# Kernel optimization log

Hardware: AMD Instinct MI355X
Metric: run time of the kernel (lower is better)

The kernel has to match this reference:

```python
import jax, jax.numpy as jnp
import numpy as np

N = 20000      # nodes
E = 320000     # edges (avg degree 16)
DIN = 50       # PPI input features
C = 121        # PPI classes
HID = 1024     # 4 heads x 256 concatenated
H3 = 6         # heads in last layer


def setup_inputs() -> dict:
    key = jax.random.key(0)
    ks = jax.random.split(key, 7)
    X = jax.random.normal(ks[0], (N, DIN), jnp.float32)
    edge_index = jax.random.randint(ks[1], (2, E), 0, N, dtype=jnp.int32)
    def w(k, i, o):
        return jax.random.normal(k, (i, o), jnp.float32) / jnp.sqrt(jnp.float32(i))
    return {
        "X": X,
        "edge_index": edge_index,
        "W1": w(ks[2], DIN, HID),        # 4 heads x 256, concatenated
        "W2": w(ks[3], HID, HID),        # 4 heads x 256 GCN weights
        "S2": w(ks[4], HID, HID),        # 4 heads x 256 skip linears
        "W3": w(ks[5], HID, H3 * C),     # 6 heads x num_classes GCN weights
        "S3": w(ks[6], HID, H3 * C),     # 6 heads x num_classes skip linears
    }


def _agg(xw, row, col, norm, n):
    # GCN symmetric-normalized neighbor sum: out[col] += norm * xw[row]
    return jax.ops.segment_sum(xw[row] * norm[:, None], col, num_segments=n)


def reference(X, edge_index, W1, W2, S2, W3, S3):
    n = X.shape[0]
    row, col = edge_index[0], edge_index[1]
    # degree at targets (add_self_loops=False), D^{-1/2} A D^{-1/2} normalization
    deg = jax.ops.segment_sum(jnp.ones(row.shape, X.dtype), col, num_segments=n)
    dis = jnp.where(deg > 0, deg ** -0.5, 0.0)
    norm = dis[row] * dis[col]
    # layer 1: 4 GCN heads (weights concatenated), elu, concat
    h1 = jax.nn.elu(_agg(X @ W1, row, col, norm, n))              # [N, 1024]
    # layer 2: 4 GCN heads + linear skip, elu, concat
    h2 = jax.nn.elu(_agg(h1 @ W2, row, col, norm, n) + h1 @ S2)   # [N, 1024]
    # layer 3: 6 GCN heads + linear skip, average over heads (Identity act)
    y = _agg(h2 @ W3, row, col, norm, n) + h2 @ S3                # [N, 6*C]
    return y.reshape(n, H3, C).mean(axis=1)                       # [N, C]
```

## Files before the change

kernel.cpp:

```cpp
#include <hip/hip_runtime.h>
#include <hip/hip_bf16.h>
#include <math.h>

#define N_NODES 20000
#define N_EDGES 320000
#define DIN 50
#define HID 1024
#define NC3 726
#define NCLS 121
#define KCAT 2048
#define NQ 242

typedef __attribute__((ext_vector_type(8))) _Float16 half8;
typedef __attribute__((ext_vector_type(4))) float floatx4;

__device__ __forceinline__ unsigned short f2h(float v) {
    _Float16 h = (_Float16)v;
    return __builtin_bit_cast(unsigned short, h);
}
__device__ __forceinline__ float h2f(unsigned short u) {
    return (float)__builtin_bit_cast(_Float16, u);
}

__device__ __forceinline__ void async16(const void* g, void* l) {
    __builtin_amdgcn_global_load_lds(
        (const __attribute__((address_space(1))) void*)g,
        (__attribute__((address_space(3))) void*)l,
        16, 0, 0);
}


__global__ void zero_int_kernel(int* p, int n) {
    int i = blockIdx.x * blockDim.x + threadIdx.x;
    if (i < n) p[i] = 0;
}

__global__ __launch_bounds__(1024) void scan_kernel(const int* __restrict__ deg,
                                                    int* __restrict__ offs,
                                                    int* __restrict__ cursor,
                                                    float* __restrict__ dis,
                                                    int n, int total) {
    __shared__ int part[1024];
    int t = threadIdx.x;
    const int CH = (n + 1023) / 1024;
    int base0 = t * CH;
    int s = 0;
    for (int i = 0; i < CH; ++i) {
        int idx = base0 + i;
        if (idx < n) s += deg[idx];
    }
    part[t] = s;
    __syncthreads();
    for (int d = 1; d < 1024; d <<= 1) {
        int v = (t >= d) ? part[t - d] : 0;
        __syncthreads();
        part[t] += v;
        __syncthreads();
    }
    int run = part[t] - s;
    for (int i = 0; i < CH; ++i) {
        int idx = base0 + i;
        if (idx < n) {
            int d = deg[idx];
            offs[idx] = run;
            cursor[idx] = run;
            dis[idx] = d > 0 ? rsqrtf((float)d) : 0.0f;
            run += d;
        }
    }
    if (t == 1023) offs[n] = total;
}

__global__ void scatter_kernel(const int* __restrict__ row, const int* __restrict__ col,
                               const float* __restrict__ dis, int* __restrict__ cursor,
                               int* __restrict__ csr_src, float* __restrict__ csr_w, int e) {
    int i = blockIdx.x * blockDim.x + threadIdx.x;
    if (i < e) {
        int r = row[i], c = col[i];
        float nm = dis[r] * dis[c];
        int pos = atomicAdd(&cursor[c], 1);
        csr_src[pos] = r;
        csr_w[pos] = nm;
    }
}

__global__ __launch_bounds__(256) void prep_kernel(const int* __restrict__ ecol,
                                                   int* __restrict__ deg,
                                                   const float* __restrict__ W1,
                                                   unsigned short* __restrict__ Bt1,
                                                   const float* __restrict__ W2,
                                                   const float* __restrict__ S2,
                                                   unsigned short* __restrict__ Bt2,
                                                   const float* __restrict__ W3,
                                                   const float* __restrict__ S3,
                                                   unsigned short* __restrict__ Bt3) {
    __shared__ unsigned short tile[32][33];
    const int b = blockIdx.x;
    const int tid = threadIdx.x;

    if (b < 2048) {
        int src = b >> 10;
        int t = b & 1023;
        int k0 = (t >> 5) * 32;
        int n0 = (t & 31) * 32;
        const float* W = src ? S2 : W2;
        int koff = src ? HID : 0;
        int tx = tid & 31;
        int ty = tid >> 5;
#pragma unroll
        for (int r = 0; r < 32; r += 8)
            tile[ty + r][tx] = f2h(W[(size_t)(k0 + ty + r) * HID + n0 + tx]);
        __syncthreads();
#pragma unroll
        for (int r = 0; r < 32; r += 8)
            Bt2[(size_t)(n0 + ty + r) * KCAT + koff + k0 + tx] = tile[tx][ty + r];
    } else if (b < 2304) {
        int tb = b - 2048;
        int src = tb >> 7;
        int t = tb & 127;
        int k0 = (t >> 2) * 32;
        int c0 = (t & 3) * 32;
        const float* W = src ? S3 : W3;
        int tx = tid & 31;
        int ty = tid >> 5;
#pragma unroll
        for (int r = 0; r < 32; r += 8) {
            int k = k0 + ty + r, c = c0 + tx;
            float v = 0.0f;
            if (c < NCLS) {
                const float* p = W + (size_t)k * NC3 + c;
                v = (p[0] + p[121] + p[242] + p[363] + p[484] + p[605]) * (1.0f / 6.0f);
            }
            tile[ty + r][tx] = f2h(v);
        }
        __syncthreads();
#pragma unroll
        for (int r = 0; r < 32; r += 8) {
            int c = c0 + ty + r;
            if (c < NCLS)
                Bt3[(size_t)(src * NCLS + c) * HID + k0 + tx] = tile[tx][ty + r];
        }
    } else if (b < 2560) {
        int i = (b - 2304) * 256 + tid;
        int n = i / 64, k = i - n * 64;
        Bt1[i] = (k < DIN) ? f2h(W1[(size_t)k * HID + n]) : (unsigned short)0;
    } else {
        int i = (b - 2560) * 256 + tid;
        if (i < N_EDGES) atomicAdd(&deg[ecol[i]], 1);
    }
}


__global__ __launch_bounds__(64) void aggX_kernel(const float* __restrict__ X,
                                                  const int* __restrict__ offs,
                                                  const int* __restrict__ csr_src,
                                                  const float* __restrict__ csr_w,
                                                  unsigned short* __restrict__ gX) {
    int n = blockIdx.x;
    int t = threadIdx.x;
    float a = 0.0f;
    if (t < DIN) {
        int p0 = offs[n], p1 = offs[n + 1];
        for (int p = p0; p < p1; ++p) {
            a = fmaf(csr_w[p], X[(size_t)csr_src[p] * DIN + t], a);
        }
    }
    gX[(size_t)n * 64 + t] = (t < DIN) ? f2h(a) : (unsigned short)0;
}

__global__ __launch_bounds__(256) void agg_slice_kernel(const unsigned short* __restrict__ h,
                                                        const int* __restrict__ offs,
                                                        const int* __restrict__ csr_src,
                                                        const float* __restrict__ csr_w,
                                                        unsigned short* __restrict__ g) {
    const int f = blockIdx.x;
    const int slice = f & 7;
    const int nb = f >> 3;
    const int tid = threadIdx.x;
    const int n = nb * 16 + (tid >> 4);
    const int coloff = slice * 128 + (tid & 15) * 8;
    const unsigned short* hp = h + coloff;

    float a[8] = {0, 0, 0, 0, 0, 0, 0, 0};
    int p0 = offs[n], p1 = offs[n + 1];
    for (int p = p0; p < p1; ++p) {
        int s = csr_src[p];
        float w = csr_w[p];
        uint4 v = *(const uint4*)&hp[(size_t)s * HID];
        const unsigned short* vs = (const unsigned short*)&v;
#pragma unroll
        for (int j = 0; j < 8; ++j) a[j] = fmaf(w, h2f(vs[j]), a[j]);
    }
    unsigned short ov[8];
#pragma unroll
    for (int j = 0; j < 8; ++j) ov[j] = f2h(a[j]);
    *(uint4*)&g[(size_t)n * HID + coloff] = *(const uint4*)ov;
}

__global__ __launch_bounds__(256) void agg3_kernel(const unsigned short* __restrict__ Q,
                                                   const int* __restrict__ offs,
                                                   const int* __restrict__ csr_src,
                                                   const float* __restrict__ csr_w,
                                                   float* __restrict__ out) {
    int n = blockIdx.x * 2 + (threadIdx.x >> 7);
    int c = threadIdx.x & 127;
    if (c >= NCLS) return;
    float a = 0.0f;
    int p0 = offs[n], p1 = offs[n + 1];
    for (int p = p0; p < p1; ++p) {
        a = fmaf(csr_w[p], h2f(Q[(size_t)csr_src[p] * NQ + c]), a);
    }
    a += h2f(Q[(size_t)n * NQ + NCLS + c]);
    out[(size_t)n * NCLS + c] = a;
}


#define GBM 128
#define GBN 128
#define GBK 32

template <int EPI>
__global__ __launch_bounds__(256, 4) void mfma_gemm_kernel(
        const unsigned short* __restrict__ Ag, const unsigned short* __restrict__ Ah,
        const unsigned short* __restrict__ Bt,
        void* __restrict__ Co,
        int M, int N, int ldc, int ktot, int khalf, int kw,
        int NB, int MB, int mchunk) {
    __shared__ __align__(16) unsigned short sA[2][GBM * GBK];
    __shared__ __align__(16) unsigned short sB[2][GBN * GBK];

    const int f = blockIdx.x;
    const int xcd = f & 7;
    const int r0 = f >> 3;
    const int nB = r0 % NB;
    const int mi = r0 / NB;
    const int mB = xcd * mchunk + mi;
    if (mB >= MB) return;
    const int bm = mB * GBM;
    const int bn = nB * GBN;
    const int ks = blockIdx.y;

    const int tid = threadIdx.x;
    const int lane = tid & 63;
    const int wave = tid >> 6;
    const int wm = wave >> 1;
    const int wn = wave & 1;

    const int st_r = tid >> 2;
    const int st_slot = tid & 3;
    const int st_c = (st_slot ^ ((st_r >> 1) & 3)) * 8;
    const int st_lds = st_r * GBK + st_slot * 8;

    int agm[2], bgn[2];
#pragma unroll
    for (int p = 0; p < 2; ++p) {
        int gm = bm + st_r + p * 64;
        agm[p] = gm < M ? gm : M - 1;
        int gn = bn + st_r + p * 64;
        bgn[p] = gn < N ? gn : N - 1;
    }

    const int frow = lane & 15;
    const int fkc = (((lane >> 4) ^ ((frow >> 1) & 3))) * 8;

    floatx4 acc[4][4];
#pragma unroll
    for (int i = 0; i < 4; ++i)
#pragma unroll
        for (int j = 0; j < 4; ++j) acc[i][j] = (floatx4){0.f, 0.f, 0.f, 0.f};

    auto issue = [&](int k0, int buf) {
        const unsigned short* ap = (k0 < khalf) ? Ag : Ah;
        int ka = (k0 < khalf) ? k0 : k0 - khalf;
#pragma unroll
        for (int p = 0; p < 2; ++p) {
            async16(&ap[(size_t)agm[p] * khalf + ka + st_c],
                    &sA[buf][p * 64 * GBK + st_lds]);
            async16(&Bt[(size_t)bgn[p] * ktot + k0 + st_c],
                    &sB[buf][p * 64 * GBK + st_lds]);
        }
    };

    const int tw = kw / GBK;
    const int t0 = ks * tw;
    const int t1 = t0 + tw;

    issue(t0 * GBK, 0);

    for (int t = t0; t < t1; ++t) {
        __syncthreads();
        if (t + 1 < t1) issue((t + 1) * GBK, (t + 1) & 1);

        const unsigned short* a_base = sA[t & 1];
        const unsigned short* b_base = sB[t & 1];
        half8 fa[4], fb[4];
#pragma unroll
        for (int i = 0; i < 4; ++i)
            fa[i] = *(const half8*)&a_base[(wm * 64 + i * 16 + frow) * GBK + fkc];
#pragma unroll
        for (int j = 0; j < 4; ++j)
            fb[j] = *(const half8*)&b_base[(wn * 64 + j * 16 + frow) * GBK + fkc];
#pragma unroll
        for (int i = 0; i < 4; ++i)
#pragma unroll
            for (int j = 0; j < 4; ++j)
                acc[i][j] = __builtin_amdgcn_mfma_f32_16x16x32_f16(fa[i], fb[j], acc[i][j], 0, 0, 0);
    }

    const int c_r0 = (lane >> 4) * 4;
    const int c_c = lane & 15;
#pragma unroll
    for (int i = 0; i < 4; ++i)
#pragma unroll
        for (int j = 0; j < 4; ++j) {
            int gn = bn + wn * 64 + j * 16 + c_c;
            if (gn >= N) continue;
#pragma unroll
            for (int r = 0; r < 4; ++r) {
                int gm = bm + wm * 64 + i * 16 + c_r0 + r;
                if (gm >= M) continue;
                float v = acc[i][j][r];
                if (EPI == 0) {
                    v = v > 0 ? v : expf(v) - 1.0f;
                    ((unsigned short*)Co)[(size_t)gm * ldc + gn] = f2h(v);
                } else if (EPI == 1) {
                    atomicAdd(&((float*)Co)[(size_t)gm * ldc + gn], v);
                } else {
                    ((unsigned short*)Co)[(size_t)gm * ldc + gn] = f2h(v);
                }
            }
        }
}


#define BM8 256
#define BN8 256
#define BK8 64

__global__ __launch_bounds__(512, 2) void gemm8p_kernel(
        const unsigned short* __restrict__ Ag, const unsigned short* __restrict__ Ah,
        const unsigned short* __restrict__ Bt,
        unsigned short* __restrict__ Co,
        int M, int N, int ldc, int ktot, int khalf, int NBn) {
    __shared__ __align__(16) unsigned short sA[2][BM8 * BK8];
    __shared__ __align__(16) unsigned short sB[2][BN8 * BK8];

    const int nwg = gridDim.x;
    const int orig = blockIdx.x;
    const int q = nwg >> 3, r = nwg & 7;
    const int xcd = orig & 7;
    const int wg = (xcd < r ? xcd * (q + 1) : r * (q + 1) + (xcd - r) * q) + (orig >> 3);
    const int mB = wg / NBn;
    const int nB = wg - mB * NBn;
    const int bm = mB * BM8;
    const int bn = nB * BN8;

    const int tid = threadIdx.x;
    const int lane = tid & 63;
    const int wave = tid >> 6;
    const int wm = wave >> 2;
    const int wn = wave & 3;

    const int srow = tid >> 3;
    const int sslot = tid & 7;
    const int swcol = (sslot ^ (srow & 7)) * 8;
    const int ldso = srow * BK8 + sslot * 8;

    size_t aoff[4], boff[4];
#pragma unroll
    for (int rr = 0; rr < 4; ++rr) {
        int gm = bm + rr * 64 + srow; if (gm >= M) gm = M - 1;
        aoff[rr] = (size_t)gm * khalf + swcol;
        int gn = bn + rr * 64 + srow; if (gn >= N) gn = N - 1;
        boff[rr] = (size_t)gn * ktot + swcol;
    }

    auto stage_b = [&](int t, int h) {
        const int k0 = t * BK8;
        unsigned short* dst = sB[t & 1];
        async16(Bt + boff[2 * h] + k0,     dst + (2 * h) * 64 * BK8 + ldso);
        async16(Bt + boff[2 * h + 1] + k0, dst + (2 * h + 1) * 64 * BK8 + ldso);
    };
    auto stage_a = [&](int t, int w) {
        const int k0 = t * BK8;
        const unsigned short* ap = (k0 < khalf) ? Ag : Ah;
        const int ka = (k0 < khalf) ? k0 : k0 - khalf;
        unsigned short* dst = sA[t & 1];
        async16(ap + aoff[w] + ka,     dst + w * 64 * BK8 + ldso);
        async16(ap + aoff[w + 2] + ka, dst + (w + 2) * 64 * BK8 + ldso);
    };

    floatx4 acc[8][4];
#pragma unroll
    for (int i = 0; i < 8; ++i)
#pragma unroll
        for (int j = 0; j < 4; ++j) acc[i][j] = (floatx4){0.f, 0.f, 0.f, 0.f};

    const int NT = ktot / BK8;
    const int frow = lane & 15;
    const int fgrp = lane >> 4;
    const int coff0 = ((fgrp)     ^ (frow & 7)) * 8;
    const int coff1 = ((4 + fgrp) ^ (frow & 7)) * 8;

    stage_b(0, 0); stage_b(0, 1); stage_a(0, 0); stage_a(0, 1);
    asm volatile("s_waitcnt vmcnt(2)" ::: "memory");
    __builtin_amdgcn_s_barrier();

    for (int t = 0; t < NT; ++t) {
        const unsigned short* ab = sA[t & 1];
        const unsigned short* bb = sB[t & 1];
        const bool pf = (t + 1 < NT);
        half8 fa[4][2], fb[4][2];

#pragma unroll
        for (int j = 0; j < 4; ++j) {
            fb[j][0] = *(const half8*)&bb[(wn * 64 + j * 16 + frow) * BK8 + coff0];
            fb[j][1] = *(const half8*)&bb[(wn * 64 + j * 16 + frow) * BK8 + coff1];
        }
#pragma unroll
        for (int i = 0; i < 4; ++i) {
            fa[i][0] = *(const half8*)&ab[(wm * 128 + i * 16 + frow) * BK8 + coff0];
            fa[i][1] = *(const half8*)&ab[(wm * 128 + i * 16 + frow) * BK8 + coff1];
        }
        if (pf) stage_b(t + 1, 0);
        __builtin_amdgcn_s_barrier();
        __builtin_amdgcn_s_setprio(1);
#pragma unroll
        for (int kk = 0; kk < 2; ++kk)
#pragma unroll
            for (int i = 0; i < 4; ++i)
#pragma unroll
                for (int j = 0; j < 2; ++j)
                    acc[i][j] = __builtin_amdgcn_mfma_f32_16x16x32_f16(fa[i][kk], fb[j][kk], acc[i][j], 0, 0, 0);
        __builtin_amdgcn_s_setprio(0);
        __builtin_amdgcn_s_barrier();

        if (pf) stage_b(t + 1, 1);
        __builtin_amdgcn_s_barrier();
        __builtin_amdgcn_s_setprio(1);
#pragma unroll
        for (int kk = 0; kk < 2; ++kk)
#pragma unroll
            for (int i = 0; i < 4; ++i)
#pragma unroll
                for (int j = 2; j < 4; ++j)
                    acc[i][j] = __builtin_amdgcn_mfma_f32_16x16x32_f16(fa[i][kk], fb[j][kk], acc[i][j], 0, 0, 0);
        __builtin_amdgcn_s_setprio(0);
        if (pf) { asm volatile("s_waitcnt vmcnt(4)" ::: "memory"); }
        else    { asm volatile("s_waitcnt vmcnt(0)" ::: "memory"); }
        __builtin_amdgcn_s_barrier();

#pragma unroll
        for (int i = 0; i < 4; ++i) {
            fa[i][0] = *(const half8*)&ab[(wm * 128 + 64 + i * 16 + frow) * BK8 + coff0];
            fa[i][1] = *(const half8*)&ab[(wm * 128 + 64 + i * 16 + frow) * BK8 + coff1];
        }
        if (pf) stage_a(t + 1, 0);
        __builtin_amdgcn_s_barrier();
        __builtin_amdgcn_s_setprio(1);
#pragma unroll
        for (int kk = 0; kk < 2; ++kk)
#pragma unroll
            for (int i = 0; i < 4; ++i)
#pragma unroll
                for (int j = 2; j < 4; ++j)
                    acc[4 + i][j] = __builtin_amdgcn_mfma_f32_16x16x32_f16(fa[i][kk], fb[j][kk], acc[4 + i][j], 0, 0, 0);
        __builtin_amdgcn_s_setprio(0);
        __builtin_amdgcn_s_barrier();

        if (pf) stage_a(t + 1, 1);
        __builtin_amdgcn_s_barrier();
        __builtin_amdgcn_s_setprio(1);
#pragma unroll
        for (int kk = 0; kk < 2; ++kk)
#pragma unroll
            for (int i = 0; i < 4; ++i)
#pragma unroll
                for (int j = 0; j < 2; ++j)
                    acc[4 + i][j] = __builtin_amdgcn_mfma_f32_16x16x32_f16(fa[i][kk], fb[j][kk], acc[4 + i][j], 0, 0, 0);
        __builtin_amdgcn_s_setprio(0);
        if (pf) { asm volatile("s_waitcnt vmcnt(2)" ::: "memory"); }
        __builtin_amdgcn_s_barrier();
    }

    const int c_c = lane & 15;
    const int c_r0 = fgrp * 4;
#pragma unroll
    for (int i = 0; i < 8; ++i)
#pragma unroll
        for (int j = 0; j < 4; ++j) {
            const int gn = bn + wn * 64 + j * 16 + c_c;
            if (gn >= N) continue;
#pragma unroll
            for (int rr = 0; rr < 4; ++rr) {
                const int gm = bm + wm * 128 + i * 16 + c_r0 + rr;
                if (gm >= M) continue;
                float v = acc[i][j][rr];
                v = v > 0 ? v : expf(v) - 1.0f;
                Co[(size_t)gm * ldc + gn] = f2h(v);
            }
        }
}


static inline size_t align_up(size_t x, size_t a) { return (x + a - 1) & ~(a - 1); }

extern "C" void kernel_launch(void* const* d_in, const int* in_sizes, int n_in,
                              void* d_out, int out_size, void* d_ws, size_t ws_size,
                              hipStream_t stream) {
    const float* X  = (const float*)d_in[0];
    const int* erow = (const int*)d_in[1];
    const int* ecol = (const int*)d_in[1] + N_EDGES;
    const float* W1 = (const float*)d_in[2];
    const float* W2 = (const float*)d_in[3];
    const float* S2 = (const float*)d_in[4];
    const float* W3 = (const float*)d_in[5];
    const float* S3 = (const float*)d_in[6];
    float* out = (float*)d_out;

    char* w = (char*)d_ws;
    int* deg     = (int*)w;             w += align_up((size_t)N_NODES * 4, 256);
    int* offs    = (int*)w;             w += align_up((size_t)(N_NODES + 1) * 4, 256);
    int* cursor  = (int*)w;             w += align_up((size_t)N_NODES * 4, 256);
    int* csr_src = (int*)w;             w += align_up((size_t)N_EDGES * 4, 256);
    float* dis   = (float*)w;           w += align_up((size_t)N_NODES * 4, 256);
    float* csr_w = (float*)w;           w += align_up((size_t)N_EDGES * 4, 256);
    unsigned short* gXh = (unsigned short*)w; w += align_up((size_t)N_NODES * 64 * 2, 256);
    unsigned short* h1 = (unsigned short*)w;  w += align_up((size_t)N_NODES * HID * 2, 256);
    unsigned short* g  = (unsigned short*)w;  w += align_up((size_t)N_NODES * HID * 2, 256);
    unsigned short* h2 = (unsigned short*)w;  w += align_up((size_t)N_NODES * HID * 2, 256);
    unsigned short* Qh = (unsigned short*)w;  w += align_up((size_t)N_NODES * NQ * 2, 256);
    unsigned short* Bt1 = (unsigned short*)w; w += align_up((size_t)HID * 64 * 2, 256);
    unsigned short* Bt2 = (unsigned short*)w; w += align_up((size_t)HID * KCAT * 2, 256);
    unsigned short* Bt3 = (unsigned short*)w; w += align_up((size_t)NQ * HID * 2, 256);

    const int TB = 256;
    int nb_n = (N_NODES + TB - 1) / TB;

    zero_int_kernel<<<nb_n, TB, 0, stream>>>(deg, N_NODES);
    prep_kernel<<<3810, 256, 0, stream>>>(ecol, deg, W1, Bt1, W2, S2, Bt2, W3, S3, Bt3);

    scan_kernel<<<1, 1024, 0, stream>>>(deg, offs, cursor, dis, N_NODES, N_EDGES);
    scatter_kernel<<<(N_EDGES + TB - 1) / TB, TB, 0, stream>>>(erow, ecol, dis, cursor,
                                                               csr_src, csr_w, N_EDGES);

    const int MB = (N_NODES + GBM - 1) / GBM;
    const int mchunk = (MB + 7) / 8;
    const int NB2 = HID / GBN;
    const int NB3 = (NQ + GBN - 1) / GBN;
    const int AGG_GRID = 8 * (N_NODES / 16);

    const int MB8 = (N_NODES + BM8 - 1) / BM8;
    const int NB8 = HID / BN8;

    aggX_kernel<<<N_NODES, 64, 0, stream>>>(X, offs, csr_src, csr_w, gXh);
    mfma_gemm_kernel<0><<<dim3(8 * mchunk * NB2, 1), 256, 0, stream>>>(
        gXh, gXh, Bt1, h1, N_NODES, HID, HID, 64, 64, 64, NB2, MB, mchunk);

    agg_slice_kernel<<<AGG_GRID, 256, 0, stream>>>(h1, offs, csr_src, csr_w, g);
    gemm8p_kernel<<<dim3(MB8 * NB8), 512, 0, stream>>>(
        g, h1, Bt2, h2, N_NODES, HID, HID, KCAT, HID, NB8);

    mfma_gemm_kernel<2><<<dim3(8 * mchunk * NB3, 1), 256, 0, stream>>>(
        h2, h2, Bt3, Qh, N_NODES, NQ, NQ, HID, HID, HID, NB3, MB, mchunk);
    agg3_kernel<<<N_NODES / 2, 256, 0, stream>>>(Qh, offs, csr_src, csr_w, out);
}
```

Measured before the change: 504.3 us.

## Coarsen GEMM main-loop phases from four to two with fewer barriers

Restructures the double-buffered GEMM K-loop so each iteration issues both halves of the next B tile, then both halves of the next A tile, as single batches. This cuts the four MFMA phases to two and removes several workgroup barriers per iteration. Fewer barriers cost less sync and give longer MFMA runs. In exchange, global loads are issued in larger bursts and interleave less finely with compute. The B prefetch now starts before the current B fragments are read from the other buffer, which relies on double buffering for correctness.

```diff
diff --git a/kernel.cpp b/kernel.cpp
--- a/kernel.cpp
+++ b/kernel.cpp
@@ -412,6 +412,7 @@
         const bool pf = (t + 1 < NT);
         half8 fa[4][2], fb[4][2];
 
+        if (pf) { stage_b(t + 1, 0); stage_b(t + 1, 1); }
 #pragma unroll
         for (int j = 0; j < 4; ++j) {
             fb[j][0] = *(const half8*)&bb[(wn * 64 + j * 16 + frow) * BK8 + coff0];
@@ -422,65 +423,38 @@
             fa[i][0] = *(const half8*)&ab[(wm * 128 + i * 16 + frow) * BK8 + coff0];
             fa[i][1] = *(const half8*)&ab[(wm * 128 + i * 16 + frow) * BK8 + coff1];
         }
-        if (pf) stage_b(t + 1, 0);
-        __builtin_amdgcn_s_barrier();
         __builtin_amdgcn_s_setprio(1);
 #pragma unroll
         for (int kk = 0; kk < 2; ++kk)
 #pragma unroll
             for (int i = 0; i < 4; ++i)
 #pragma unroll
-                for (int j = 0; j < 2; ++j)
-                    acc[i][j] = __builtin_amdgcn_mfma_f32_16x16x32_f16(fa[i][kk], fb[j][kk], acc[i][j], 0, 0, 0);
-        __builtin_amdgcn_s_setprio(0);
-        __builtin_amdgcn_s_barrier();
-
-        if (pf) stage_b(t + 1, 1);
-        __builtin_amdgcn_s_barrier();
-        __builtin_amdgcn_s_setprio(1);
-#pragma unroll
-        for (int kk = 0; kk < 2; ++kk)
-#pragma unroll
-            for (int i = 0; i < 4; ++i)
-#pragma unroll
-                for (int j = 2; j < 4; ++j)
+                for (int j = 0; j < 4; ++j)
                     acc[i][j] = __builtin_amdgcn_mfma_f32_16x16x32_f16(fa[i][kk], fb[j][kk], acc[i][j], 0, 0, 0);
         __builtin_amdgcn_s_setprio(0);
         if (pf) { asm volatile("s_waitcnt vmcnt(4)" ::: "memory"); }
         else    { asm volatile("s_waitcnt vmcnt(0)" ::: "memory"); }
         __builtin_amdgcn_s_barrier();
 
+        if (pf) { stage_a(t + 1, 0); stage_a(t + 1, 1); }
 #pragma unroll
         for (int i = 0; i < 4; ++i) {
             fa[i][0] = *(const half8*)&ab[(wm * 128 + 64 + i * 16 + frow) * BK8 + coff0];
             fa[i][1] = *(const half8*)&ab[(wm * 128 + 64 + i * 16 + frow) * BK8 + coff1];
         }
-        if (pf) stage_a(t + 1, 0);
-        __builtin_amdgcn_s_barrier();
         __builtin_amdgcn_s_setprio(1);
 #pragma unroll
         for (int kk = 0; kk < 2; ++kk)
 #pragma unroll
             for (int i = 0; i < 4; ++i)
 #pragma unroll
-                for (int j = 2; j < 4; ++j)
+                for (int j = 0; j < 4; ++j)
                     acc[4 + i][j] = __builtin_amdgcn_mfma_f32_16x16x32_f16(fa[i][kk], fb[j][kk], acc[4 + i][j], 0, 0, 0);
         __builtin_amdgcn_s_setprio(0);
-        __builtin_amdgcn_s_barrier();
-
-        if (pf) stage_a(t + 1, 1);
-        __builtin_amdgcn_s_barrier();
-        __builtin_amdgcn_s_setprio(1);
-#pragma unroll
-        for (int kk = 0; kk < 2; ++kk)
-#pragma unroll
-            for (int i = 0; i < 4; ++i)
-#pragma unroll
-                for (int j = 0; j < 2; ++j)
-                    acc[4 + i][j] = __builtin_amdgcn_mfma_f32_16x16x32_f16(fa[i][kk], fb[j][kk], acc[4 + i][j], 0, 0, 0);
-        __builtin_amdgcn_s_setprio(0);
-        if (pf) { asm volatile("s_waitcnt vmcnt(2)" ::: "memory"); }
-        __builtin_amdgcn_s_barrier();
+        if (pf) {
+            asm volatile("s_waitcnt vmcnt(2)" ::: "memory");
+            __builtin_amdgcn_s_barrier();
+        }
     }
 
     const int c_c = lane & 15;
```

Result: slower. 536.5 us (+6.4%).
